# Performance work log

Measured on AMD Instinct MI355X. Metric: run time of the kernel, lower is better.

Reference implementation:

```python
import jax, jax.numpy as jnp
from jax import lax
import numpy as np

DILATIONS = (6, 12, 18, 24)
NCLS = 21
NIT = 4


def setup_inputs() -> dict:
    key = jax.random.key(0)
    ks = jax.random.split(key, 8)
    bs, cin, w, h = 8, 2048, 32, 32
    x = jax.random.normal(ks[0], (bs, cin, w, h), dtype=jnp.float32)
    diffW = jax.random.uniform(ks[1], (bs, w * h, w * h), dtype=jnp.float32)
    # per-branch params (stacked over the NIT=4 dilation branches)
    conv2d_w = 0.01 * jax.random.normal(ks[2], (NIT, 1024, cin, 3, 3), dtype=jnp.float32)
    conv2d_b = 0.01 * jax.random.normal(ks[3], (NIT, 1024), dtype=jnp.float32)
    conv1_w = 0.01 * jax.random.normal(ks[4], (NIT, NCLS, 1024, 1, 1), dtype=jnp.float32)
    conv1_b = 0.01 * jax.random.normal(ks[5], (NIT, NCLS), dtype=jnp.float32)
    pool_w = jnp.full((NIT, 1, NCLS), 5.0, dtype=jnp.float32)  # weiPooling weights, torch init ones*5
    return {"x": x, "diffW": diffW, "conv2d_w": conv2d_w, "conv2d_b": conv2d_b,
            "conv1_w": conv1_w, "conv1_b": conv1_b, "pool_w": pool_w}


def reference(x, diffW, conv2d_w, conv2d_b, conv1_w, conv1_b, pool_w):
    bs, _, w, h = x.shape
    wh = w * h
    # threshold + row-normalize adjacency, then transpose (original builds diag(1/rowsum) @ diffW per sample)
    dW = jnp.where(diffW > 0.8, diffW, 0.0)
    dWn = (dW / dW.sum(axis=2, keepdims=True)).transpose(0, 2, 1)  # [bs, wh, wh]

    out_diff_all = []
    wei_cum = jnp.zeros((bs, NCLS, wh), dtype=x.dtype)
    for it in range(NIT):
        d = DILATIONS[it]
        out = lax.conv_general_dilated(
            x, conv2d_w[it], window_strides=(1, 1), padding=[(d, d), (d, d)],
            rhs_dilation=(d, d), dimension_numbers=("NCHW", "OIHW", "NCHW"))
        out = out + conv2d_b[it][None, :, None, None]  # [bs, 1024, w, h]
        out_diff_all.append(out)
        # diffusion aggregation: feat @ diffW_norm
        od = jnp.einsum("bdn,bnm->bdm", out.reshape(bs, 1024, wh), dWn)  # [bs, 1024, wh]
        # 1x1 conv (stride 1) as matmul
        o2 = jnp.einsum("bdn,cd->bcn", od, conv1_w[it][:, :, 0, 0]) + conv1_b[it][None, :, None]
        wei_cum = wei_cum + o2 / NIT

    wei_cum = jax.nn.softmax(wei_cum, axis=1)

    prob = jnp.zeros((bs, NCLS), dtype=x.dtype)
    wei = None
    for it in range(NIT):
        # weiPooling: softmax over classes again, then softmax over spatial dim of scaled weights
        inp = jax.nn.softmax(wei_cum, axis=1)
        wei = jax.nn.softmax(inp * jnp.exp(pool_w[it][0])[None, :, None], axis=2)  # [bs, ncls, wh]
        pooled = jnp.einsum("bcn,bdn->bcd", wei, out_diff_all[it].reshape(bs, 1024, wh))  # [bs, ncls, 1024]
        # pred_sw: elementwise product with 1x1-conv weight, sum over features, add bias
        pred = (pooled * conv1_w[it][:, :, 0, 0][None]).sum(2) + conv1_b[it][None, :]
        prob = prob + pred / NIT

    prob = jax.nn.sigmoid(prob).reshape(bs, 1, NCLS)
    return (prob, wei_cum, wei)
```

## Files before the change

### kernel.cpp

```cpp
#include <hip/hip_runtime.h>
#include <hip/hip_bf16.h>

typedef unsigned short u16;
typedef __attribute__((ext_vector_type(4))) float f32x4;
typedef __attribute__((ext_vector_type(4))) int i32x4;
typedef __attribute__((ext_vector_type(8))) short bf16x8;

#define NIT 4
#define NCLS 21
#define BS 8
#define CIN 2048
#define COUT 1024
#define WH 1024

#define SX 32.0f
#define SW 3200.0f
#define INVS (1.0f / (SX * SW))

__device__ __forceinline__ u16 f2bf(float f) {
  union { float f; unsigned u; } v; v.f = f;
  unsigned r = v.u + 0x7fffu + ((v.u >> 16) & 1u);
  return (u16)(r >> 16);
}
__device__ __forceinline__ float bf2f(u16 h) {
  union { unsigned u; float f; } v; v.u = ((unsigned)h) << 16;
  return v.f;
}
__device__ __forceinline__ signed char q8(float v, float s) {
  float x = v * s;
  x = fminf(fmaxf(x, -127.f), 127.f);
  return (signed char)__float2int_rn(x);
}

#define GLDS16(gp, lp) __builtin_amdgcn_global_load_lds( \
    (const __attribute__((address_space(1))) unsigned int*)(gp), \
    (__attribute__((address_space(3))) unsigned int*)(lp), 16, 0, 0)

__global__ void prep_w_kernel(const float* __restrict__ w, signed char* __restrict__ wt) {
  int it = blockIdx.x >> 10, co = blockIdx.x & 1023;
  const float* src = w + (size_t)(it * 1024 + co) * (CIN * 9);
  __shared__ float ls[2304];
  int t = threadIdx.x;
  for (int chunk = 0; chunk < 8; ++chunk) {
    for (int i = t; i < 2304; i += 256) ls[i] = src[chunk * 2304 + i];
    __syncthreads();
    #pragma unroll
    for (int tap = 0; tap < 9; ++tap) {
      float v = ls[t * 9 + tap];
      wt[(((size_t)(it * 9 + tap) * 1024 + co) * CIN) + chunk * 256 + t] = q8(v, SW);
    }
    __syncthreads();
  }
}

__global__ void prep_x_kernel(const float* __restrict__ x, signed char* __restrict__ xT) {
  int bid = blockIdx.x;
  int pT = bid & 15, ciT = (bid >> 4) & 31, b = bid >> 9;
  __shared__ float ls[64][65];
  int t = threadIdx.x;
  int tr = t >> 6, tc = t & 63;
  const float* xp = x + ((size_t)b * CIN + ciT * 64) * WH + pT * 64;
  #pragma unroll
  for (int r = 0; r < 16; ++r) {
    int ci = r * 4 + tr;
    ls[ci][tc] = xp[(size_t)ci * WH + tc];
  }
  __syncthreads();
  signed char* xtp = xT + ((size_t)b * WH + pT * 64) * CIN + ciT * 64;
  #pragma unroll
  for (int r = 0; r < 16; ++r) {
    int p = r * 4 + tr;
    xtp[(size_t)p * CIN + tc] = q8(ls[tc][p], SX);
  }
}

__global__ void norm_kernel(const float* __restrict__ diffW, u16* __restrict__ normT) {
  int b = blockIdx.x >> 10, m = blockIdx.x & 1023;
  const float* row = diffW + ((size_t)(b * 1024 + m)) * 1024;
  int t = threadIdx.x;
  float v[4]; float s = 0.f;
  #pragma unroll
  for (int i = 0; i < 4; ++i) {
    float x = row[t + i * 256];
    x = (x > 0.8f) ? x : 0.f;
    v[i] = x; s += x;
  }
  #pragma unroll
  for (int off = 1; off < 64; off <<= 1) s += __shfl_xor(s, off);
  __shared__ float red[4];
  if ((t & 63) == 0) red[t >> 6] = s;
  __syncthreads();
  float inv = 1.f / (red[0] + red[1] + red[2] + red[3]);
  u16* orow = normT + ((size_t)(b * 1024 + m)) * 1024;
  #pragma unroll
  for (int i = 0; i < 4; ++i) orow[t + i * 256] = f2bf(v[i] * inv);
}

__global__ void zero_kernel(float* p) { p[threadIdx.x] = 0.f; }

__global__ __launch_bounds__(512, 2)
void conv8_kernel(const signed char* __restrict__ wt, const signed char* __restrict__ xT,
                  const float* __restrict__ bias, const signed char* __restrict__ zpage,
                  u16* __restrict__ out_all) {
  const int bid = blockIdx.x;
  const int b = bid & 7;
  const int s = bid >> 3;
  const int g = s >> 2, mt = s & 3;
  const int it = g >> 2;
  const int nt = (int)((0x2130321030213210ULL >> (g * 4)) & 0xFULL);
  const int M0 = mt * 256, N0 = nt * 256;
  const int tid = threadIdx.x, wave = tid >> 6, lane = tid & 63;
  const int wm = wave >> 2, wn = wave & 3;

  const int dil = 6 * (it + 1);
  const int tlo = (8 * nt + 7 < dil) ? 3 : 0;
  const int thi = (8 * nt + dil >= 32) ? 6 : 9;
  const int NT = (thi - tlo) * 16;

  __shared__ char lds[2][2][256][128];

  const signed char* Aglob = wt + (size_t)it * 9 * COUT * CIN;
  const signed char* Bglob = xT + (size_t)b * WH * CIN;

  const int srow = lane >> 3;
  const int scol16 = (lane & 7) ^ srow;

  const signed char* abase[4]; const signed char* bbase[4];
  unsigned long long vmask = 0ull;
  #pragma unroll
  for (int r = 0; r < 4; ++r) {
    int arow = M0 + r * 64 + wave * 8 + srow;
    abase[r] = Aglob + (size_t)arow * CIN + scol16 * 16;
    int n = N0 + r * 64 + wave * 8 + srow;
    bbase[r] = Bglob + (size_t)n * CIN + scol16 * 16;
    int py0 = n >> 5, px0 = n & 31;
    #pragma unroll
    for (int tap = 0; tap < 9; ++tap) {
      int t3 = (tap * 11) >> 5;
      int py = py0 + (t3 - 1) * dil;
      int px = px0 + (tap - t3 * 3 - 1) * dil;
      if (((unsigned)py < 32u) && ((unsigned)px < 32u))
        vmask |= (1ull << (r * 9 + tap));
    }
  }
  const signed char* zp = zpage + scol16 * 16;

  auto stageA = [&](int jj, int hf, int bb) {
    if (jj >= NT) return;
    int tap = tlo + (jj >> 4);
    size_t uoff = (size_t)tap * (COUT * CIN) + (size_t)((jj & 15) << 7);
    #pragma unroll
    for (int i = 0; i < 2; ++i) {
      int r = hf * 2 + i;
      GLDS16(abase[r] + uoff, &lds[bb][0][hf * 128 + i * 64 + wave * 8][0]);
    }
  };
  auto stageB = [&](int jj, int hf, int bb) {
    if (jj >= NT) return;
    int tap = tlo + (jj >> 4);
    int t3 = (tap * 11) >> 5;
    ptrdiff_t toff = (ptrdiff_t)(((t3 - 1) * 32 + (tap - t3 * 3 - 1)) * dil) * CIN
                   + (ptrdiff_t)((jj & 15) << 7);
    #pragma unroll
    for (int i = 0; i < 2; ++i) {
      int r = hf * 2 + i;
      bool valid = (vmask >> (r * 9 + tap)) & 1ull;
      const signed char* src = valid ? (bbase[r] + toff) : zp;
      GLDS16(src, &lds[bb][1][hf * 128 + i * 64 + wave * 8][0]);
    }
  };

  i32x4 acc[8][4] = {};

  const int l15 = lane & 15;
  const int colx[2] = { (((lane >> 4) ^ (lane & 7)) * 16),
                        (((4 + (lane >> 4)) ^ (lane & 7)) * 16) };
  const int arow_byte = (wm * 128 + l15) * 128;
  const int brow_byte = (wn * 64 + l15) * 128;

  stageA(0, 0, 0); stageA(0, 1, 0);
  stageB(0, 0, 0); stageB(0, 1, 0);
  __builtin_amdgcn_sched_barrier(0);
  asm volatile("s_waitcnt vmcnt(0)" ::: "memory");
  __builtin_amdgcn_s_barrier();
  __builtin_amdgcn_sched_barrier(0);

  for (int j = 0; j < NT; ++j) {
    const int p2 = j & 1;
    const char* Ab = (const char*)&lds[p2][0][0][0];
    const char* Bb = (const char*)&lds[p2][1][0][0];

    i32x4 bfr[4][2];
    #pragma unroll
    for (int nf = 0; nf < 4; ++nf) {
      bfr[nf][0] = *(const i32x4*)(Bb + brow_byte + nf * 2048 + colx[0]);
      bfr[nf][1] = *(const i32x4*)(Bb + brow_byte + nf * 2048 + colx[1]);
    }
    stageA(j + 1, 0, p2 ^ 1);
    stageA(j + 1, 1, p2 ^ 1);
    stageB(j + 1, 0, p2 ^ 1);
    stageB(j + 1, 1, p2 ^ 1);

    __builtin_amdgcn_s_setprio(1);
    #pragma unroll
    for (int m = 0; m < 8; ++m) {
      i32x4 a0 = *(const i32x4*)(Ab + arow_byte + m * 2048 + colx[0]);
      i32x4 a1 = *(const i32x4*)(Ab + arow_byte + m * 2048 + colx[1]);
      #pragma unroll
      for (int nf = 0; nf < 4; ++nf) {
        acc[m][nf] = __builtin_amdgcn_mfma_i32_16x16x64_i8(a0, bfr[nf][0], acc[m][nf], 0, 0, 0);
        acc[m][nf] = __builtin_amdgcn_mfma_i32_16x16x64_i8(a1, bfr[nf][1], acc[m][nf], 0, 0, 0);
      }
    }
    __builtin_amdgcn_s_setprio(0);
    __builtin_amdgcn_sched_barrier(0);
    asm volatile("s_waitcnt vmcnt(0)" ::: "memory");
    __builtin_amdgcn_s_barrier();
    __builtin_amdgcn_sched_barrier(0);
  }

  u16* outp = out_all + (size_t)(it * BS + b) * COUT * WH;
  const float* bias_it = bias + it * COUT;
  #pragma unroll
  for (int mf = 0; mf < 8; ++mf)
    #pragma unroll
    for (int nf = 0; nf < 4; ++nf) {
      int col = N0 + wn * 64 + nf * 16 + l15;
      #pragma unroll
      for (int r = 0; r < 4; ++r) {
        int row = M0 + wm * 128 + mf * 16 + (lane >> 4) * 4 + r;
        float v = (float)acc[mf][nf][r] * INVS + bias_it[row];
        outp[((size_t)row << 10) + col] = f2bf(v);
      }
    }
}

__global__ __launch_bounds__(1024, 4)
void p_kernel(const u16* __restrict__ out_all, const float* __restrict__ w1,
              float* __restrict__ P) {
  int bidx = blockIdx.x;
  int kch = bidx & 3, sl = bidx >> 2;
  int it = sl >> 3;
  int t = threadIdx.x;
  int wave = t >> 6, lane = t & 63;
  int g = wave & 3;
  int k = kch * 256 + (wave >> 2) * 64 + lane;
  __shared__ float w1f[21][512];
  const u16* op = out_all + ((size_t)sl << 20) + k;
  const float* w1p = w1 + (size_t)it * NCLS * 1024;
  float acc[6] = {0.f, 0.f, 0.f, 0.f, 0.f, 0.f};
  const int cbase = g * 6;
  for (int h = 0; h < 2; ++h) {
    __syncthreads();
    for (int l = t; l < 21 * 128; l += 1024) {
      int c = l >> 7, qq = l & 127;
      *(f32x4*)&w1f[c][qq * 4] = *(const f32x4*)(w1p + (size_t)c * 1024 + h * 512 + qq * 4);
    }
    __syncthreads();
    const u16* oph = op + ((size_t)(h * 512) << 10);
    #pragma unroll 4
    for (int dq = 0; dq < 128; ++dq) {
      float vv[4];
      #pragma unroll
      for (int j = 0; j < 4; ++j) vv[j] = bf2f(oph[(size_t)(dq * 4 + j) << 10]);
      #pragma unroll
      for (int cj = 0; cj < 6; ++cj) {
        int c = cbase + cj; if (c > 20) c = 20;
        f32x4 w4 = *(const f32x4*)&w1f[c][dq * 4];
        acc[cj] = fmaf(w4[0], vv[0], acc[cj]);
        acc[cj] = fmaf(w4[1], vv[1], acc[cj]);
        acc[cj] = fmaf(w4[2], vv[2], acc[cj]);
        acc[cj] = fmaf(w4[3], vv[3], acc[cj]);
      }
    }
  }
  float* Pp = P + (((size_t)sl * NCLS) << 10) + k;
  #pragma unroll
  for (int cj = 0; cj < 6; ++cj) {
    int c = cbase + cj;
    if (c < NCLS) Pp[(size_t)c << 10] = acc[cj];
  }
}

__global__ __launch_bounds__(256, 2)
void weicum2_kernel(const float* __restrict__ P, const u16* __restrict__ normT,
                    const float* __restrict__ b1, float* __restrict__ wc_out,
                    float* __restrict__ inp) {
  int bidx = blockIdx.x;
  int mch = bidx & 3, b = bidx >> 2;
  int t = threadIdx.x;
  __shared__ u16 ps[21][1024];
  for (int l = t; l < 21 * 128; l += 256) {
    int c = l >> 7, qq = l & 127;
    float s[8] = {};
    #pragma unroll
    for (int itp = 0; itp < 4; ++itp) {
      const float* pp = P + ((((size_t)(itp * 8 + b)) * NCLS + c) << 10) + qq * 8;
      f32x4 a0 = *(const f32x4*)pp;
      f32x4 a1 = *(const f32x4*)(pp + 4);
      s[0] += a0[0]; s[1] += a0[1]; s[2] += a0[2]; s[3] += a0[3];
      s[4] += a1[0]; s[5] += a1[1]; s[6] += a1[2]; s[7] += a1[3];
    }
    bf16x8 pv;
    #pragma unroll
    for (int j = 0; j < 8; ++j) pv[j] = (short)f2bf(s[j]);
    *(bf16x8*)&ps[c][qq * 8] = pv;
  }
  __syncthreads();
  int m = mch * 256 + t;
  const u16* nr = normT + ((size_t)(b * 1024 + m)) * 1024;
  float acc[NCLS];
  #pragma unroll
  for (int c = 0; c < NCLS; ++c) acc[c] = 0.f;
  for (int oct = 0; oct < 128; ++oct) {
    bf16x8 nv = *(const bf16x8*)(nr + oct * 8);
    float nf[8];
    #pragma unroll
    for (int j = 0; j < 8; ++j) nf[j] = bf2f((u16)nv[j]);
    #pragma unroll
    for (int c = 0; c < NCLS; ++c) {
      bf16x8 pv = *(const bf16x8*)&ps[c][oct * 8];
      #pragma unroll
      for (int j = 0; j < 8; ++j) acc[c] = fmaf(nf[j], bf2f((u16)pv[j]), acc[c]);
    }
  }
  float mx = -1e30f;
  #pragma unroll
  for (int c = 0; c < NCLS; ++c) {
    float bs = 0.f;
    #pragma unroll
    for (int itp = 0; itp < NIT; ++itp) bs += b1[itp * NCLS + c];
    acc[c] = (acc[c] + bs) * 0.25f;
    mx = fmaxf(mx, acc[c]);
  }
  float s = 0.f;
  #pragma unroll
  for (int c = 0; c < NCLS; ++c) { acc[c] = expf(acc[c] - mx); s += acc[c]; }
  float inv = 1.f / s;
  float* wp = wc_out + (((size_t)b * NCLS) << 10) + m;
  float mx2 = -1e30f;
  #pragma unroll
  for (int c = 0; c < NCLS; ++c) {
    acc[c] *= inv;
    wp[(size_t)c << 10] = acc[c];
    mx2 = fmaxf(mx2, acc[c]);
  }
  float s2 = 0.f;
  #pragma unroll
  for (int c = 0; c < NCLS; ++c) { acc[c] = expf(acc[c] - mx2); s2 += acc[c]; }
  float inv2 = 1.f / s2;
  float* ip = inp + (((size_t)b * NCLS) << 10) + m;
  #pragma unroll
  for (int c = 0; c < NCLS; ++c) ip[(size_t)c << 10] = acc[c] * inv2;
}

__global__ void weipred_kernel(const float* __restrict__ inp, const float* __restrict__ proj,
                               const float* __restrict__ pool_w, const float* __restrict__ b1,
                               float* __restrict__ pred, float* __restrict__ wei_out) {
  int bid = blockIdx.x;
  int it = bid / 168, r = bid % 168;
  int b = r / NCLS, c = r % NCLS;
  int t = threadIdx.x;
  float scale = expf(pool_w[it * NCLS + c]);
  const float* ip = inp + ((size_t)(b * NCLS + c)) * 1024;
  float v[4]; float mx = -1e30f;
  #pragma unroll
  for (int i = 0; i < 4; ++i) { v[i] = ip[t + i * 256] * scale; mx = fmaxf(mx, v[i]); }
  __shared__ float red[4];
  #pragma unroll
  for (int off = 1; off < 64; off <<= 1) mx = fmaxf(mx, __shfl_xor(mx, off));
  if ((t & 63) == 0) red[t >> 6] = mx;
  __syncthreads();
  mx = fmaxf(fmaxf(red[0], red[1]), fmaxf(red[2], red[3]));
  __syncthreads();
  float s = 0.f;
  #pragma unroll
  for (int i = 0; i < 4; ++i) { v[i] = expf(v[i] - mx); s += v[i]; }
  #pragma unroll
  for (int off = 1; off < 64; off <<= 1) s += __shfl_xor(s, off);
  if ((t & 63) == 0) red[t >> 6] = s;
  __syncthreads();
  s = red[0] + red[1] + red[2] + red[3];
  float inv = 1.f / s;
  __syncthreads();
  const float* pj = proj + (((size_t)(it * BS + b)) * NCLS + c) * 1024;
  float ps = 0.f;
  #pragma unroll
  for (int i = 0; i < 4; ++i) {
    float wv = v[i] * inv;
    ps += wv * pj[t + i * 256];
    if (it == NIT - 1) wei_out[((size_t)(b * NCLS + c)) * 1024 + t + i * 256] = wv;
  }
  #pragma unroll
  for (int off = 1; off < 64; off <<= 1) ps += __shfl_xor(ps, off);
  if ((t & 63) == 0) red[t >> 6] = ps;
  __syncthreads();
  if (t == 0) pred[bid] = red[0] + red[1] + red[2] + red[3] + b1[it * NCLS + c];
}

__global__ void prob_kernel(const float* __restrict__ pred, float* __restrict__ out) {
  int i = threadIdx.x;
  if (i < BS * NCLS) {
    float s = 0.f;
    #pragma unroll
    for (int it = 0; it < NIT; ++it) s += pred[it * BS * NCLS + i];
    s *= 0.25f;
    out[i] = 1.f / (1.f + expf(-s));
  }
}

extern "C" void kernel_launch(void* const* d_in, const int* in_sizes, int n_in,
                              void* d_out, int out_size, void* d_ws, size_t ws_size,
                              hipStream_t stream) {
  const float* x        = (const float*)d_in[0];
  const float* diffW    = (const float*)d_in[1];
  const float* conv2d_w = (const float*)d_in[2];
  const float* conv2d_b = (const float*)d_in[3];
  const float* conv1_w  = (const float*)d_in[4];
  const float* conv1_b  = (const float*)d_in[5];
  const float* pool_w   = (const float*)d_in[6];
  float* out = (float*)d_out;

  char* ws = (char*)d_ws;
  signed char* wt      = (signed char*)(ws);
  signed char* xT      = (signed char*)(ws + 75497472);
  u16*         normT   = (u16*)(ws + 92274688);
  u16*         out_all = (u16*)(ws + 109051904);
  float*       P       = (float*)(ws + 176160768);
  float*       inp     = (float*)(ws + 187170816);
  float*       pred    = (float*)(ws + 187858944);
  float*       zpage   = (float*)(ws + 187861632);

  float* out_prob = out;
  float* out_wc   = out + 168;
  float* out_wei  = out + 168 + 172032;

  hipLaunchKernelGGL(zero_kernel, dim3(1), dim3(256), 0, stream, zpage);
  hipLaunchKernelGGL(prep_w_kernel, dim3(4096), dim3(256), 0, stream, conv2d_w, wt);
  hipLaunchKernelGGL(prep_x_kernel, dim3(4096), dim3(256), 0, stream, x, xT);
  hipLaunchKernelGGL(norm_kernel, dim3(8192), dim3(256), 0, stream, diffW, normT);
  hipLaunchKernelGGL(conv8_kernel, dim3(512), dim3(512), 0, stream,
                     wt, xT, conv2d_b, (const signed char*)zpage, out_all);
  hipLaunchKernelGGL(p_kernel, dim3(128), dim3(1024), 0, stream, out_all, conv1_w, P);
  hipLaunchKernelGGL(weicum2_kernel, dim3(32), dim3(256), 0, stream,
                     P, normT, conv1_b, out_wc, inp);
  hipLaunchKernelGGL(weipred_kernel, dim3(672), dim3(256), 0, stream,
                     inp, P, pool_w, conv1_b, pred, out_wei);
  hipLaunchKernelGGL(prob_kernel, dim3(1), dim3(256), 0, stream, pred, out_prob);
}
```

Before: 738.6 us.

## Vectorize prep kernels and split weicum reduction across more blocks

```diff
diff --git a/kernel.cpp b/kernel.cpp
--- a/kernel.cpp
+++ b/kernel.cpp
@@ -26,34 +26,42 @@
   union { unsigned u; float f; } v; v.u = ((unsigned)h) << 16;
   return v.f;
 }
-__device__ __forceinline__ signed char q8(float v, float s) {
+__device__ __forceinline__ unsigned q8u(float v, float s) {
   float x = v * s;
   x = fminf(fmaxf(x, -127.f), 127.f);
-  return (signed char)__float2int_rn(x);
+  return (unsigned)(unsigned char)(signed char)__float2int_rn(x);
 }
 
 #define GLDS16(gp, lp) __builtin_amdgcn_global_load_lds( \
     (const __attribute__((address_space(1))) unsigned int*)(gp), \
     (__attribute__((address_space(3))) unsigned int*)(lp), 16, 0, 0)
 
-__global__ void prep_w_kernel(const float* __restrict__ w, signed char* __restrict__ wt) {
+__global__ void prep_w_kernel(const float* __restrict__ w, unsigned* __restrict__ wt4) {
   int it = blockIdx.x >> 10, co = blockIdx.x & 1023;
-  const float* src = w + (size_t)(it * 1024 + co) * (CIN * 9);
-  __shared__ float ls[2304];
-  int t = threadIdx.x;
-  for (int chunk = 0; chunk < 8; ++chunk) {
-    for (int i = t; i < 2304; i += 256) ls[i] = src[chunk * 2304 + i];
+  const f32x4* src4 = (const f32x4*)(w + (size_t)(it * 1024 + co) * (CIN * 9));
+  __shared__ float ls[9216];
+  int t = threadIdx.x;
+  for (int chunk = 0; chunk < 2; ++chunk) {
+    for (int i = t; i < 2304; i += 256)
+      *(f32x4*)&ls[i * 4] = src4[chunk * 2304 + i];
     __syncthreads();
+    float r[36];
+    #pragma unroll
+    for (int j = 0; j < 9; ++j)
+      *(f32x4*)&r[j * 4] = *(const f32x4*)&ls[t * 36 + j * 4];
     #pragma unroll
     for (int tap = 0; tap < 9; ++tap) {
-      float v = ls[t * 9 + tap];
-      wt[(((size_t)(it * 9 + tap) * 1024 + co) * CIN) + chunk * 256 + t] = q8(v, SW);
+      unsigned pk = q8u(r[tap], SW)
+                  | (q8u(r[9 + tap], SW) << 8)
+                  | (q8u(r[18 + tap], SW) << 16)
+                  | (q8u(r[27 + tap], SW) << 24);
+      wt4[((((size_t)(it * 9 + tap) * 1024 + co) * CIN + chunk * 1024) >> 2) + t] = pk;
     }
     __syncthreads();
   }
 }
 
-__global__ void prep_x_kernel(const float* __restrict__ x, signed char* __restrict__ xT) {
+__global__ void prep_x_kernel(const float* __restrict__ x, unsigned* __restrict__ xT4) {
   int bid = blockIdx.x;
   int pT = bid & 15, ciT = (bid >> 4) & 31, b = bid >> 9;
   __shared__ float ls[64][65];
@@ -66,24 +74,29 @@
     ls[ci][tc] = xp[(size_t)ci * WH + tc];
   }
   __syncthreads();
-  signed char* xtp = xT + ((size_t)b * WH + pT * 64) * CIN + ciT * 64;
-  #pragma unroll
-  for (int r = 0; r < 16; ++r) {
-    int p = r * 4 + tr;
-    xtp[(size_t)p * CIN + tc] = q8(ls[tc][p], SX);
+  unsigned* xtp = xT4 + ((((size_t)b * WH + pT * 64) * CIN + ciT * 64) >> 2);
+  #pragma unroll
+  for (int r = 0; r < 4; ++r) {
+    int p = r * 16 + (t >> 4);
+    int ci0 = (t & 15) * 4;
+    unsigned pk = q8u(ls[ci0][p], SX)
+                | (q8u(ls[ci0 + 1][p], SX) << 8)
+                | (q8u(ls[ci0 + 2][p], SX) << 16)
+                | (q8u(ls[ci0 + 3][p], SX) << 24);
+    xtp[(size_t)p * (CIN >> 2) + (t & 15)] = pk;
   }
 }
 
 __global__ void norm_kernel(const float* __restrict__ diffW, u16* __restrict__ normT) {
   int b = blockIdx.x >> 10, m = blockIdx.x & 1023;
-  const float* row = diffW + ((size_t)(b * 1024 + m)) * 1024;
-  int t = threadIdx.x;
-  float v[4]; float s = 0.f;
+  int t = threadIdx.x;
+  const f32x4* row4 = (const f32x4*)(diffW + (((size_t)(b * 1024 + m)) << 10));
+  f32x4 vv = row4[t];
+  float s = 0.f;
   #pragma unroll
   for (int i = 0; i < 4; ++i) {
-    float x = row[t + i * 256];
-    x = (x > 0.8f) ? x : 0.f;
-    v[i] = x; s += x;
+    vv[i] = (vv[i] > 0.8f) ? vv[i] : 0.f;
+    s += vv[i];
   }
   #pragma unroll
   for (int off = 1; off < 64; off <<= 1) s += __shfl_xor(s, off);
@@ -91,9 +104,10 @@
   if ((t & 63) == 0) red[t >> 6] = s;
   __syncthreads();
   float inv = 1.f / (red[0] + red[1] + red[2] + red[3]);
-  u16* orow = normT + ((size_t)(b * 1024 + m)) * 1024;
-  #pragma unroll
-  for (int i = 0; i < 4; ++i) orow[t + i * 256] = f2bf(v[i] * inv);
+  ushort4 o;
+  o.x = f2bf(vv[0] * inv); o.y = f2bf(vv[1] * inv);
+  o.z = f2bf(vv[2] * inv); o.w = f2bf(vv[3] * inv);
+  *((ushort4*)(normT + (((size_t)(b * 1024 + m)) << 10)) + t) = o;
 }
 
 __global__ void zero_kernel(float* p) { p[threadIdx.x] = 0.f; }
@@ -235,16 +249,16 @@
     }
 }
 
-__global__ __launch_bounds__(1024, 4)
+__global__ __launch_bounds__(512, 2)
 void p_kernel(const u16* __restrict__ out_all, const float* __restrict__ w1,
               float* __restrict__ P) {
   int bidx = blockIdx.x;
-  int kch = bidx & 3, sl = bidx >> 2;
+  int kch = bidx & 7, sl = bidx >> 3;
   int it = sl >> 3;
   int t = threadIdx.x;
   int wave = t >> 6, lane = t & 63;
   int g = wave & 3;
-  int k = kch * 256 + (wave >> 2) * 64 + lane;
+  int k = kch * 128 + (wave >> 2) * 64 + lane;
   __shared__ float w1f[21][512];
   const u16* op = out_all + ((size_t)sl << 20) + k;
   const float* w1p = w1 + (size_t)it * NCLS * 1024;
@@ -252,7 +266,7 @@
   const int cbase = g * 6;
   for (int h = 0; h < 2; ++h) {
     __syncthreads();
-    for (int l = t; l < 21 * 128; l += 1024) {
+    for (int l = t; l < 21 * 128; l += 512) {
       int c = l >> 7, qq = l & 127;
       *(f32x4*)&w1f[c][qq * 4] = *(const f32x4*)(w1p + (size_t)c * 1024 + h * 512 + qq * 4);
     }
@@ -282,37 +296,45 @@
   }
 }
 
-__global__ __launch_bounds__(256, 2)
-void weicum2_kernel(const float* __restrict__ P, const u16* __restrict__ normT,
-                    const float* __restrict__ b1, float* __restrict__ wc_out,
-                    float* __restrict__ inp) {
+__global__ void psum_kernel(const float* __restrict__ P, u16* __restrict__ Psum) {
+  int idx = blockIdx.x * 256 + threadIdx.x;
+  int k8 = idx & 127;
+  int c = (idx >> 7) % 21;
+  int b = idx / (21 * 128);
+  float s[8] = {};
+  #pragma unroll
+  for (int it = 0; it < 4; ++it) {
+    const float* pp = P + ((((size_t)(it * 8 + b)) * NCLS + c) << 10) + k8 * 8;
+    f32x4 a0 = *(const f32x4*)pp;
+    f32x4 a1 = *(const f32x4*)(pp + 4);
+    s[0] += a0[0]; s[1] += a0[1]; s[2] += a0[2]; s[3] += a0[3];
+    s[4] += a1[0]; s[5] += a1[1]; s[6] += a1[2]; s[7] += a1[3];
+  }
+  bf16x8 pv;
+  #pragma unroll
+  for (int j = 0; j < 8; ++j) pv[j] = (short)f2bf(s[j]);
+  *(bf16x8*)(Psum + (((size_t)(b * NCLS + c)) << 10) + k8 * 8) = pv;
+}
+
+__global__ __launch_bounds__(256, 4)
+void weicum2a_kernel(const u16* __restrict__ Psum, const u16* __restrict__ normT,
+                     float* __restrict__ o2part) {
   int bidx = blockIdx.x;
-  int mch = bidx & 3, b = bidx >> 2;
-  int t = threadIdx.x;
-  __shared__ u16 ps[21][1024];
-  for (int l = t; l < 21 * 128; l += 256) {
-    int c = l >> 7, qq = l & 127;
-    float s[8] = {};
-    #pragma unroll
-    for (int itp = 0; itp < 4; ++itp) {
-      const float* pp = P + ((((size_t)(itp * 8 + b)) * NCLS + c) << 10) + qq * 8;
-      f32x4 a0 = *(const f32x4*)pp;
-      f32x4 a1 = *(const f32x4*)(pp + 4);
-      s[0] += a0[0]; s[1] += a0[1]; s[2] += a0[2]; s[3] += a0[3];
-      s[4] += a1[0]; s[5] += a1[1]; s[6] += a1[2]; s[7] += a1[3];
-    }
-    bf16x8 pv;
-    #pragma unroll
-    for (int j = 0; j < 8; ++j) pv[j] = (short)f2bf(s[j]);
-    *(bf16x8*)&ps[c][qq * 8] = pv;
+  int kch = bidx & 3, mch = (bidx >> 2) & 3, b = bidx >> 4;
+  int t = threadIdx.x;
+  __shared__ u16 ps[21][256];
+  for (int l = t; l < 21 * 32; l += 256) {
+    int c = l >> 5, q = l & 31;
+    *(bf16x8*)&ps[c][q * 8] =
+        *(const bf16x8*)(Psum + (((size_t)(b * NCLS + c)) << 10) + kch * 256 + q * 8);
   }
   __syncthreads();
   int m = mch * 256 + t;
-  const u16* nr = normT + ((size_t)(b * 1024 + m)) * 1024;
+  const u16* nr = normT + ((size_t)(b * 1024 + m)) * 1024 + kch * 256;
   float acc[NCLS];
   #pragma unroll
   for (int c = 0; c < NCLS; ++c) acc[c] = 0.f;
-  for (int oct = 0; oct < 128; ++oct) {
+  for (int oct = 0; oct < 32; ++oct) {
     bf16x8 nv = *(const bf16x8*)(nr + oct * 8);
     float nf[8];
     #pragma unroll
@@ -323,6 +345,26 @@
       #pragma unroll
       for (int j = 0; j < 8; ++j) acc[c] = fmaf(nf[j], bf2f((u16)pv[j]), acc[c]);
     }
+  }
+  float* op = o2part + (size_t)bidx * NCLS * 256;
+  #pragma unroll
+  for (int c = 0; c < NCLS; ++c) op[c * 256 + t] = acc[c];
+}
+
+__global__ void weicum2b_kernel(const float* __restrict__ o2part, const float* __restrict__ b1,
+                                float* __restrict__ wc_out, float* __restrict__ inp) {
+  int bidx = blockIdx.x;
+  int mch = bidx & 3, b = bidx >> 2;
+  int t = threadIdx.x;
+  int m = mch * 256 + t;
+  float acc[NCLS];
+  #pragma unroll
+  for (int c = 0; c < NCLS; ++c) {
+    float s = 0.f;
+    #pragma unroll
+    for (int kch = 0; kch < 4; ++kch)
+      s += o2part[((size_t)((b * 4 + mch) * 4 + kch) * NCLS + c) * 256 + t];
+    acc[c] = s;
   }
   float mx = -1e30f;
   #pragma unroll
@@ -427,23 +469,30 @@
   u16*         normT   = (u16*)(ws + 92274688);
   u16*         out_all = (u16*)(ws + 109051904);
   float*       P       = (float*)(ws + 176160768);
-  float*       inp     = (float*)(ws + 187170816);
-  float*       pred    = (float*)(ws + 187858944);
-  float*       zpage   = (float*)(ws + 187861632);
+  u16*         Psum    = (u16*)(ws + 187170816);
+  float*       o2part  = (float*)(ws + 187514880);
+  float*       inp     = (float*)(ws + 190267392);
+  float*       pred    = (float*)(ws + 190955520);
+  float*       zpage   = (float*)(ws + 190958208);
 
   float* out_prob = out;
   float* out_wc   = out + 168;
   float* out_wei  = out + 168 + 172032;
 
   hipLaunchKernelGGL(zero_kernel, dim3(1), dim3(256), 0, stream, zpage);
-  hipLaunchKernelGGL(prep_w_kernel, dim3(4096), dim3(256), 0, stream, conv2d_w, wt);
-  hipLaunchKernelGGL(prep_x_kernel, dim3(4096), dim3(256), 0, stream, x, xT);
+  hipLaunchKernelGGL(prep_w_kernel, dim3(4096), dim3(256), 0, stream,
+                     conv2d_w, (unsigned*)wt);
+  hipLaunchKernelGGL(prep_x_kernel, dim3(4096), dim3(256), 0, stream,
+                     x, (unsigned*)xT);
   hipLaunchKernelGGL(norm_kernel, dim3(8192), dim3(256), 0, stream, diffW, normT);
   hipLaunchKernelGGL(conv8_kernel, dim3(512), dim3(512), 0, stream,
                      wt, xT, conv2d_b, (const signed char*)zpage, out_all);
-  hipLaunchKernelGGL(p_kernel, dim3(128), dim3(1024), 0, stream, out_all, conv1_w, P);
-  hipLaunchKernelGGL(weicum2_kernel, dim3(32), dim3(256), 0, stream,
-                     P, normT, conv1_b, out_wc, inp);
+  hipLaunchKernelGGL(p_kernel, dim3(256), dim3(512), 0, stream, out_all, conv1_w, P);
+  hipLaunchKernelGGL(psum_kernel, dim3(84), dim3(256), 0, stream, P, Psum);
+  hipLaunchKernelGGL(weicum2a_kernel, dim3(128), dim3(256), 0, stream,
+                     Psum, normT, o2part);
+  hipLaunchKernelGGL(weicum2b_kernel, dim3(32), dim3(256), 0, stream,
+                     o2part, conv1_b, out_wc, inp);
   hipLaunchKernelGGL(weipred_kernel, dim3(672), dim3(256), 0, stream,
                      inp, P, pool_w, conv1_b, pred, out_wei);
   hipLaunchKernelGGL(prob_kernel, dim3(1), dim3(256), 0, stream, pred, out_prob);
```

Result: faster. 681.5 us (-7.7%).
